# Performance work log

Measured on AMD Instinct MI355X. Metric: run time of the kernel, lower is better.

Reference implementation:

```python
import jax, jax.numpy as jnp
import numpy as np

ALPHA = 0.2  # leaky_relu negative slope
NEG_INF = -1e9


def setup_inputs() -> dict:
    key = jax.random.key(0)
    ks = jax.random.split(key, 8)
    B, U, N, Din, H, HD = 8, 1024, 2048, 128, 4, 32
    return {
        "user_features": jax.random.normal(ks[0], (B, U, Din), jnp.float32),
        "news_features": jax.random.normal(ks[1], (B, N, Din), jnp.float32),
        "adjacency": jax.random.randint(ks[2], (B, U + N, U + N), 0, 2, jnp.int32),
        "W_user": jax.random.normal(ks[3], (H, Din, HD), jnp.float32) * 0.1,
        "W_news": jax.random.normal(ks[4], (H, Din, HD), jnp.float32) * 0.1,
        "a_user_news": jax.random.normal(ks[5], (H, 2 * HD, 1), jnp.float32) * 0.1,
        "a_news_user": jax.random.normal(ks[6], (H, 2 * HD, 1), jnp.float32) * 0.1,
        "b_user": jnp.zeros((H * HD,), jnp.float32),
        "b_news": jnp.zeros((H * HD,), jnp.float32),
    }


def _attention(q, k, a, mask):
    # q: (B,H,Q,hd), k: (B,H,K,hd), a: (H,2*hd,1), mask: (B,Q,K)
    # Additive score decomposed: [q;k] @ a == q@a_q + k@a_k (same math,
    # avoids materializing the (B,H,Q,K,2hd) concat tensor).
    hd = q.shape[-1]
    a_q = a[:, :hd, 0]  # (H,hd)
    a_k = a[:, hd:, 0]  # (H,hd)
    e_q = jnp.einsum("bhqd,hd->bhq", q, a_q)
    e_k = jnp.einsum("bhkd,hd->bhk", k, a_k)
    scores = e_q[..., :, None] + e_k[..., None, :]  # (B,H,Q,K)
    scores = jnp.where(scores > 0, scores, ALPHA * scores)  # leaky_relu
    scores = jnp.where(mask[:, None, :, :] > 0, scores, NEG_INF)
    return jax.nn.softmax(scores, axis=-1)


def reference(user_features, news_features, adjacency, W_user, W_news,
              a_user_news, a_news_user, b_user, b_news):
    B, U, _ = user_features.shape
    N = news_features.shape[1]
    units = b_user.shape[0]
    user_to_news = adjacency[:, :U, U:]   # (B,U,N)
    news_to_user = adjacency[:, U:, :U]   # (B,N,U)

    q_user = jnp.einsum("bud,hdk->bhuk", user_features, W_user)  # (B,H,U,hd)
    k_news = jnp.einsum("bnd,hdk->bhnk", news_features, W_news)  # (B,H,N,hd)

    attn_un = _attention(q_user, k_news, a_user_news, user_to_news)  # (B,H,U,N)
    user_updates = jnp.einsum("bhun,bhnk->bhuk", attn_un, k_news)

    attn_nu = _attention(k_news, q_user, a_news_user, news_to_user)  # (B,H,N,U)
    news_updates = jnp.einsum("bhnu,bhuk->bhnk", attn_nu, q_user)

    # concat_heads=True: original does a raw reshape of (B,H,*,hd) -> (B,*,units)
    updated_users = jnp.reshape(user_updates, (B, U, units)) + b_user
    updated_news = jnp.reshape(news_updates, (B, N, units)) + b_news
    updated_users = jax.nn.relu(updated_users)
    updated_news = jax.nn.relu(updated_news)
    return updated_users, updated_news
```

## Files before the change

### kernel.cpp

```cpp
#include <hip/hip_runtime.h>
#include <hip/hip_bf16.h>

typedef _Float16 half8 __attribute__((ext_vector_type(8)));
typedef __fp16 fp16x2 __attribute__((ext_vector_type(2)));
typedef float f32x4 __attribute__((ext_vector_type(4)));

#define B_ 8
#define U_ 1024
#define N_ 2048
#define DIN 128
#define H_ 4
#define HD 32
#define S_ 3072
#define LOG2E 1.44269504f

__global__ __launch_bounds__(256) void p1_kernel(
    const float* __restrict__ uf, const float* __restrict__ nf,
    const float* __restrict__ Wu, const float* __restrict__ Wn,
    const float* __restrict__ a_un, const float* __restrict__ a_nu,
    _Float16* __restrict__ vtA, _Float16* __restrict__ vtB,
    float* __restrict__ eRowA, float* __restrict__ eColA,
    float* __restrict__ eRowB, float* __restrict__ eColB)
{
  __shared__ float fs[64][132];
  __shared__ float WsT[32][132];
  __shared__ float qt[32][65];
  __shared__ float aAs[32], aBs[32];

  const int bid = blockIdx.x;
  const int tid = threadIdx.x;

  int b, rt, R;
  const float *feat, *W;
  _Float16* vt;
  float *eA, *eB;
  int aAoff, aBoff;
  const float *avA, *avB;
  if (bid < 128) {
    b = bid >> 4; rt = bid & 15; R = U_;
    feat = uf; W = Wu; vt = vtB;
    eA = eRowA; eB = eColB;
    avA = a_un; aAoff = 0;  avB = a_nu; aBoff = HD;
  } else {
    int t2 = bid - 128;
    b = t2 >> 5; rt = t2 & 31; R = N_;
    feat = nf; W = Wn; vt = vtA;
    eA = eColA; eB = eRowB;
    avA = a_un; aAoff = HD; avB = a_nu; aBoff = 0;
  }
  const int r0 = rt * 64;
  const float4* feat4 = (const float4*)(feat + ((size_t)b * R + r0) * DIN);
  #pragma unroll
  for (int i = 0; i < 8; ++i) {
    int f4 = tid + 256 * i;
    int row = f4 >> 5, c4 = f4 & 31;
    *(float4*)&fs[row][c4 * 4] = feat4[row * 32 + c4];
  }

  const int kk = tid & 15, uu = tid >> 4;
  const int u2 = tid & 63, part = tid >> 6;
  float eAv[H_], eBv[H_];

  #pragma unroll
  for (int h = 0; h < H_; ++h) {
    __syncthreads();
    {
      const float4* W4 = (const float4*)(W + (size_t)h * DIN * HD);
      #pragma unroll
      for (int i = 0; i < 4; ++i) {
        int f4 = tid + 256 * i;
        int d = f4 >> 3, kc = f4 & 7;
        float4 v = W4[f4];
        WsT[kc * 4 + 0][d] = v.x;
        WsT[kc * 4 + 1][d] = v.y;
        WsT[kc * 4 + 2][d] = v.z;
        WsT[kc * 4 + 3][d] = v.w;
      }
      if (tid < 32) {
        aAs[tid] = avA[h * 64 + aAoff + tid];
        aBs[tid] = avB[h * 64 + aBoff + tid];
      }
    }
    __syncthreads();
    {
      float acc0[4] = {0.f, 0.f, 0.f, 0.f}, acc1[4] = {0.f, 0.f, 0.f, 0.f};
      #pragma unroll 8
      for (int d = 0; d < DIN; d += 4) {
        float4 w0 = *(const float4*)&WsT[kk][d];
        float4 w1 = *(const float4*)&WsT[kk + 16][d];
        #pragma unroll
        for (int i = 0; i < 4; ++i) {
          float4 fv = *(const float4*)&fs[uu + 16 * i][d];
          acc0[i] = fmaf(fv.x, w0.x, acc0[i]); acc0[i] = fmaf(fv.y, w0.y, acc0[i]);
          acc0[i] = fmaf(fv.z, w0.z, acc0[i]); acc0[i] = fmaf(fv.w, w0.w, acc0[i]);
          acc1[i] = fmaf(fv.x, w1.x, acc1[i]); acc1[i] = fmaf(fv.y, w1.y, acc1[i]);
          acc1[i] = fmaf(fv.z, w1.z, acc1[i]); acc1[i] = fmaf(fv.w, w1.w, acc1[i]);
        }
      }
      #pragma unroll
      for (int i = 0; i < 4; ++i) {
        qt[kk][uu + 16 * i] = acc0[i];
        qt[kk + 16][uu + 16 * i] = acc1[i];
      }
    }
    __syncthreads();
    {
      size_t vtbase = ((size_t)(b * H_ + h) * HD) * R + r0;
      #pragma unroll
      for (int jj = 0; jj < 8; ++jj) {
        int krow = part * 8 + jj;
        vt[vtbase + (size_t)krow * R + u2] = (_Float16)qt[krow][u2];
      }
      float a_ = 0.f, b2_ = 0.f;
      #pragma unroll
      for (int k2 = 0; k2 < HD; ++k2) {
        float qv = qt[k2][u2];
        a_  = fmaf(qv, aAs[k2], a_);
        b2_ = fmaf(qv, aBs[k2], b2_);
      }
      eAv[h] = a_  * LOG2E;
      eBv[h] = b2_ * LOG2E;
    }
  }
  if (part == 0) {
    #pragma unroll
    for (int h = 0; h < H_; ++h)
      eA[(size_t)(b * H_ + h) * R + r0 + u2] = eAv[h];
  } else if (part == 1) {
    #pragma unroll
    for (int h = 0; h < H_; ++h)
      eB[(size_t)(b * H_ + h) * R + r0 + u2] = eBv[h];
  }
}

template<int RR, int CC, int ROFF, int COFF, int PAD64>
__device__ __forceinline__ void p2_core(
    int b, int rt, int wave, int l,
    const int* __restrict__ adj, const _Float16* __restrict__ vt,
    const float* __restrict__ eRow, const float* __restrict__ eCol,
    float* __restrict__ num, float* __restrict__ den,
    unsigned long long* maskU)
{
  constexpr int CW64 = CC / 64;

  const int* adjBase = adj + (size_t)b * S_ * S_ + (size_t)(ROFF + rt * 16) * S_ + COFF;
  #pragma unroll 4
  for (int i = 0; i < (16 * CW64) / 4; ++i) {
    int f = i * 4 + wave;
    int row = f / CW64, chunk = f % CW64;
    int av = adjBase[(size_t)row * S_ + chunk * 64 + l];
    unsigned long long m = __ballot(av != 0);
    if (l == 0) maskU[row * PAD64 + chunk] = m;
  }
  __syncthreads();

  const int h = wave;
  const int row16 = l & 15;
  const int cg = (l >> 4) << 3;
  const int r = rt * 16 + row16;
  const float eq = eRow[(size_t)(b * H_ + h) * RR + r];
  const float* ecolH = eCol + (size_t)(b * H_ + h) * CC;
  const _Float16* vtb = vt + (size_t)(b * H_ + h) * HD * CC;
  const unsigned int* maskW = (const unsigned int*)maskU;
  const int mrow = row16 * (PAD64 * 2);

  f32x4 acc0 = {0.f, 0.f, 0.f, 0.f}, acc1 = {0.f, 0.f, 0.f, 0.f}, accd = {0.f, 0.f, 0.f, 0.f};
  half8 ones = {(_Float16)1.f, (_Float16)1.f, (_Float16)1.f, (_Float16)1.f,
                (_Float16)1.f, (_Float16)1.f, (_Float16)1.f, (_Float16)1.f};

  #pragma unroll 4
  for (int t = 0; t < CC / 32; ++t) {
    const int cb = t * 32 + cg;
    unsigned int mb = maskW[mrow + t] >> cg;
    float4 e0 = *(const float4*)(ecolH + cb);
    float4 e1 = *(const float4*)(ecolH + cb + 4);
    float ecv[8] = {e0.x, e0.y, e0.z, e0.w, e1.x, e1.y, e1.z, e1.w};
    float wv[8];
    #pragma unroll
    for (int j = 0; j < 8; ++j) {
      float s  = eq + ecv[j];
      float ls = fmaxf(s, 0.2f * s);
      ls = (mb & (1u << j)) ? ls : -1e9f;
      wv[j] = exp2f(ls);
    }
    union { fp16x2 h2[4]; half8 h8; } uw;
    #pragma unroll
    for (int j = 0; j < 4; ++j)
      uw.h2[j] = __builtin_amdgcn_cvt_pkrtz(wv[2 * j], wv[2 * j + 1]);
    half8 w = uw.h8;
    const half8 b0 = *(const half8*)(vtb + (size_t)row16 * CC + cb);
    const half8 b1 = *(const half8*)(vtb + (size_t)(row16 + 16) * CC + cb);
    acc0 = __builtin_amdgcn_mfma_f32_16x16x32_f16(w, b0, acc0, 0, 0, 0);
    acc1 = __builtin_amdgcn_mfma_f32_16x16x32_f16(w, b1, acc1, 0, 0, 0);
    accd = __builtin_amdgcn_mfma_f32_16x16x32_f16(w, ones, accd, 0, 0, 0);
  }

  const int colk = row16;
  const int rowbase = rt * 16 + ((l >> 4) << 2);
  #pragma unroll
  for (int q = 0; q < 4; ++q) {
    int orow = rowbase + q;
    size_t o = ((size_t)(b * H_ + h) * RR + orow) * 32 + colk;
    num[o] = acc0[q];
    num[o + 16] = acc1[q];
    if (colk == 0) den[(size_t)(b * H_ + h) * RR + orow] = accd[q];
  }
}

__global__ __launch_bounds__(256, 6) void p2_kernel(
    const int* __restrict__ adj,
    const _Float16* __restrict__ vtA, const _Float16* __restrict__ vtB,
    const float* __restrict__ eRowA, const float* __restrict__ eColA,
    const float* __restrict__ eRowB, const float* __restrict__ eColB,
    float* __restrict__ numA, float* __restrict__ denA,
    float* __restrict__ numB, float* __restrict__ denB)
{
  __shared__ unsigned long long maskU[16 * 33];
  const int tid = threadIdx.x;
  const int wave = tid >> 6, l = tid & 63;
  const int bid = blockIdx.x;
  if (bid < B_ * (U_ / 16)) {
    const int b = bid >> 6, rt = bid & 63;
    p2_core<U_, N_, 0, U_, 33>(b, rt, wave, l, adj, vtA, eRowA, eColA, numA, denA, maskU);
  } else {
    const int t2 = bid - B_ * (U_ / 16);
    const int b = t2 >> 7, rt = t2 & 127;
    p2_core<N_, U_, U_, 0, 17>(b, rt, wave, l, adj, vtB, eRowB, eColB, numB, denB, maskU);
  }
}

__global__ __launch_bounds__(256) void p3_kernel(
    const float* __restrict__ numA, const float* __restrict__ denA,
    const float* __restrict__ numB, const float* __restrict__ denB,
    const float* __restrict__ bu, const float* __restrict__ bn,
    float* __restrict__ out)
{
  int idx = blockIdx.x * 256 + threadIdx.x;
  const int nU = B_ * U_ * 128;
  if (idx < nU) {
    float v = numA[idx] / denA[idx >> 5] + bu[idx & 127];
    out[idx] = v > 0.f ? v : 0.f;
  } else {
    int i2 = idx - nU;
    float v = numB[i2] / denB[i2 >> 5] + bn[i2 & 127];
    out[idx] = v > 0.f ? v : 0.f;
  }
}

extern "C" void kernel_launch(void* const* d_in, const int* in_sizes, int n_in,
                              void* d_out, int out_size, void* d_ws, size_t ws_size,
                              hipStream_t stream) {
  const float* uf  = (const float*)d_in[0];
  const float* nf  = (const float*)d_in[1];
  const int*   adj = (const int*)d_in[2];
  const float* Wu  = (const float*)d_in[3];
  const float* Wn  = (const float*)d_in[4];
  const float* aun = (const float*)d_in[5];
  const float* anu = (const float*)d_in[6];
  const float* bu  = (const float*)d_in[7];
  const float* bn  = (const float*)d_in[8];

  char* ws = (char*)d_ws;
  size_t off = 0;
  _Float16* vtA = (_Float16*)(ws + off); off += (size_t)B_ * H_ * HD * N_ * 2;
  _Float16* vtB = (_Float16*)(ws + off); off += (size_t)B_ * H_ * HD * U_ * 2;
  float* eRowA = (float*)(ws + off); off += (size_t)B_ * H_ * U_ * 4;
  float* eColA = (float*)(ws + off); off += (size_t)B_ * H_ * N_ * 4;
  float* eRowB = (float*)(ws + off); off += (size_t)B_ * H_ * N_ * 4;
  float* eColB = (float*)(ws + off); off += (size_t)B_ * H_ * U_ * 4;
  float* numA = (float*)(ws + off); off += (size_t)B_ * U_ * 128 * 4;
  float* denA = (float*)(ws + off); off += (size_t)B_ * U_ * H_ * 4;
  float* numB = (float*)(ws + off); off += (size_t)B_ * N_ * 128 * 4;
  float* denB = (float*)(ws + off); off += (size_t)B_ * N_ * H_ * 4;
  (void)off; (void)ws_size; (void)in_sizes; (void)n_in; (void)out_size;

  p1_kernel<<<384, 256, 0, stream>>>(uf, nf, Wu, Wn, aun, anu,
                                     vtA, vtB, eRowA, eColA, eRowB, eColB);
  p2_kernel<<<B_ * (U_ / 16) + B_ * (N_ / 16), 256, 0, stream>>>(
      adj, vtA, vtB, eRowA, eColA, eRowB, eColB, numA, denA, numB, denB);
  p3_kernel<<<12288, 256, 0, stream>>>(numA, denA, numB, denB, bu, bn, (float*)d_out);
}
```

Before: 144.8 us.

## Fuse normalization epilogue into attention kernel and tile value layout

Moves the division by the softmax denominator, bias add and ReLU into the attention kernel's output stage. This removes the third kernel and the intermediate numerator/denominator buffers in global memory. The transposed value buffer is also re-laid out in 32-column tiles, so each MFMA B-operand load reads a contiguous block instead of a strided row. The risk is a slightly longer epilogue in the main kernel.

```diff
diff --git a/kernel.cpp b/kernel.cpp
--- a/kernel.cpp
+++ b/kernel.cpp
@@ -105,11 +105,12 @@
     }
     __syncthreads();
     {
-      size_t vtbase = ((size_t)(b * H_ + h) * HD) * R + r0;
+      size_t vtbase = (size_t)(b * H_ + h) * (R * HD)
+                    + (size_t)((r0 >> 5) + (u2 >> 5)) * (HD * 32) + (u2 & 31);
       #pragma unroll
       for (int jj = 0; jj < 8; ++jj) {
         int krow = part * 8 + jj;
-        vt[vtbase + (size_t)krow * R + u2] = (_Float16)qt[krow][u2];
+        vt[vtbase + krow * 32] = (_Float16)qt[krow][u2];
       }
       float a_ = 0.f, b2_ = 0.f;
       #pragma unroll
@@ -138,7 +139,7 @@
     int b, int rt, int wave, int l,
     const int* __restrict__ adj, const _Float16* __restrict__ vt,
     const float* __restrict__ eRow, const float* __restrict__ eCol,
-    float* __restrict__ num, float* __restrict__ den,
+    const float* __restrict__ bias, float* __restrict__ out,
     unsigned long long* maskU)
 {
   constexpr int CW64 = CC / 64;
@@ -160,7 +161,7 @@
   const int r = rt * 16 + row16;
   const float eq = eRow[(size_t)(b * H_ + h) * RR + r];
   const float* ecolH = eCol + (size_t)(b * H_ + h) * CC;
-  const _Float16* vtb = vt + (size_t)(b * H_ + h) * HD * CC;
+  const _Float16* vtb = vt + (size_t)(b * H_ + h) * (CC * HD);
   const unsigned int* maskW = (const unsigned int*)maskU;
   const int mrow = row16 * (PAD64 * 2);
 
@@ -188,8 +189,8 @@
     for (int j = 0; j < 4; ++j)
       uw.h2[j] = __builtin_amdgcn_cvt_pkrtz(wv[2 * j], wv[2 * j + 1]);
     half8 w = uw.h8;
-    const half8 b0 = *(const half8*)(vtb + (size_t)row16 * CC + cb);
-    const half8 b1 = *(const half8*)(vtb + (size_t)(row16 + 16) * CC + cb);
+    const half8 b0 = *(const half8*)(vtb + t * (HD * 32) + row16 * 32 + cg);
+    const half8 b1 = *(const half8*)(vtb + t * (HD * 32) + (row16 + 16) * 32 + cg);
     acc0 = __builtin_amdgcn_mfma_f32_16x16x32_f16(w, b0, acc0, 0, 0, 0);
     acc1 = __builtin_amdgcn_mfma_f32_16x16x32_f16(w, b1, acc1, 0, 0, 0);
     accd = __builtin_amdgcn_mfma_f32_16x16x32_f16(w, ones, accd, 0, 0, 0);
@@ -201,9 +202,11 @@
   for (int q = 0; q < 4; ++q) {
     int orow = rowbase + q;
     size_t o = ((size_t)(b * H_ + h) * RR + orow) * 32 + colk;
-    num[o] = acc0[q];
-    num[o + 16] = acc1[q];
-    if (colk == 0) den[(size_t)(b * H_ + h) * RR + orow] = accd[q];
+    float den = accd[q];
+    float v0 = acc0[q] / den + bias[q * 32 + colk];
+    float v1 = acc1[q] / den + bias[q * 32 + colk + 16];
+    out[o]      = v0 > 0.f ? v0 : 0.f;
+    out[o + 16] = v1 > 0.f ? v1 : 0.f;
   }
 }
 
@@ -212,8 +215,8 @@
     const _Float16* __restrict__ vtA, const _Float16* __restrict__ vtB,
     const float* __restrict__ eRowA, const float* __restrict__ eColA,
     const float* __restrict__ eRowB, const float* __restrict__ eColB,
-    float* __restrict__ numA, float* __restrict__ denA,
-    float* __restrict__ numB, float* __restrict__ denB)
+    const float* __restrict__ bu, const float* __restrict__ bn,
+    float* __restrict__ out)
 {
   __shared__ unsigned long long maskU[16 * 33];
   const int tid = threadIdx.x;
@@ -221,29 +224,13 @@
   const int bid = blockIdx.x;
   if (bid < B_ * (U_ / 16)) {
     const int b = bid >> 6, rt = bid & 63;
-    p2_core<U_, N_, 0, U_, 33>(b, rt, wave, l, adj, vtA, eRowA, eColA, numA, denA, maskU);
+    p2_core<U_, N_, 0, U_, 33>(b, rt, wave, l, adj, vtA, eRowA, eColA, bu,
+                               out, maskU);
   } else {
     const int t2 = bid - B_ * (U_ / 16);
     const int b = t2 >> 7, rt = t2 & 127;
-    p2_core<N_, U_, U_, 0, 17>(b, rt, wave, l, adj, vtB, eRowB, eColB, numB, denB, maskU);
-  }
-}
-
-__global__ __launch_bounds__(256) void p3_kernel(
-    const float* __restrict__ numA, const float* __restrict__ denA,
-    const float* __restrict__ numB, const float* __restrict__ denB,
-    const float* __restrict__ bu, const float* __restrict__ bn,
-    float* __restrict__ out)
-{
-  int idx = blockIdx.x * 256 + threadIdx.x;
-  const int nU = B_ * U_ * 128;
-  if (idx < nU) {
-    float v = numA[idx] / denA[idx >> 5] + bu[idx & 127];
-    out[idx] = v > 0.f ? v : 0.f;
-  } else {
-    int i2 = idx - nU;
-    float v = numB[i2] / denB[i2 >> 5] + bn[i2 & 127];
-    out[idx] = v > 0.f ? v : 0.f;
+    p2_core<N_, U_, U_, 0, 17>(b, rt, wave, l, adj, vtB, eRowB, eColB, bn,
+                               out + (size_t)B_ * U_ * 128, maskU);
   }
 }
 
@@ -268,15 +255,10 @@
   float* eColA = (float*)(ws + off); off += (size_t)B_ * H_ * N_ * 4;
   float* eRowB = (float*)(ws + off); off += (size_t)B_ * H_ * N_ * 4;
   float* eColB = (float*)(ws + off); off += (size_t)B_ * H_ * U_ * 4;
-  float* numA = (float*)(ws + off); off += (size_t)B_ * U_ * 128 * 4;
-  float* denA = (float*)(ws + off); off += (size_t)B_ * U_ * H_ * 4;
-  float* numB = (float*)(ws + off); off += (size_t)B_ * N_ * 128 * 4;
-  float* denB = (float*)(ws + off); off += (size_t)B_ * N_ * H_ * 4;
   (void)off; (void)ws_size; (void)in_sizes; (void)n_in; (void)out_size;
 
   p1_kernel<<<384, 256, 0, stream>>>(uf, nf, Wu, Wn, aun, anu,
                                      vtA, vtB, eRowA, eColA, eRowB, eColB);
   p2_kernel<<<B_ * (U_ / 16) + B_ * (N_ / 16), 256, 0, stream>>>(
-      adj, vtA, vtB, eRowA, eColA, eRowB, eColB, numA, denA, numB, denB);
-  p3_kernel<<<12288, 256, 0, stream>>>(numA, denA, numB, denB, bu, bn, (float*)d_out);
-}
+      adj, vtA, vtB, eRowA, eColA, eRowB, eColB, bu, bn, (float*)d_out);
+}
```

Result: faster. 139.9 us (-3.3%).
